# Kernel tuning notes

Hardware: AMD Instinct MI355X
Metric: run time of the kernel (lower is better)

The kernel has to match this reference:

```python
import jax, jax.numpy as jnp
import numpy as np

T, N, C, L, H, NL = 32, 16, 64, 64, 128, 128
NA = 2 * L              # action logits come from the K gather -> 2*L slots
TOTAL = 3 + H + NA + L  # packed RecurrentState width: a,p,v,h,a_probs,p_probs


def _gru_cell(x, h, Wih, Whh, bih, bhh):
    # PyTorch GRUCell math
    gi = x @ Wih.T + bih
    gh = h @ Whh.T + bhh
    i_r, i_z, i_n = jnp.split(gi, 3, axis=-1)
    h_r, h_z, h_n = jnp.split(gh, 3, axis=-1)
    r = jax.nn.sigmoid(i_r + h_r)
    z = jax.nn.sigmoid(i_z + h_z)
    n = jnp.tanh(i_n + r * h_n)
    return (1.0 - z) * n + z * h


def _gru_seq(xs, Wih, Whh, bih, bhh):
    # xs: (steps, B, H) -> outputs (steps, B, H), zero initial state (torch default)
    h0 = jnp.zeros((xs.shape[1], Whh.shape[1]), xs.dtype)
    def step(h, x):
        hn = _gru_cell(x, h, Wih, Whh, bih, bhh)
        return hn, hn
    _, out = jax.lax.scan(step, h0, xs)
    return out


def _forward(cond, rnn_hxs, emb, aemb, tg_Wih_f, tg_Whh_f, tg_bih_f, tg_bhh_f, tg_Wih_b, tg_Whh_b, tg_bih_b, tg_bhh_b, gc_Wih, gc_Whh, gc_bih, gc_bhh, f_W0, f_b0, f_W1, f_b1, f_W2, f_b2, c_W0, c_b0, c_W1, c_b1, c_W2, c_b2, a_W0, a_b0, a_W1, a_b1, a_Wc, a_bc, lines_obs, given_a, given_p):
    relu = jax.nn.relu
    hx = rnn_hxs[0]                       # (N, TOTAL): a(1) p(1) v(1) h(H) a_probs(NA) p_probs(L)
    h0 = hx[:, 3:3 + H]
    a_init = hx[:, 0].astype(jnp.int32)   # A[-1] = hx.a (zeros at episode start)

    # --- bidirectional task encoder over all L cyclic rolls of line embeddings ---
    M = emb[lines_obs[0]]                 # (N, L, H); only t=0 lines are used
    gi = jnp.transpose(M, (1, 0, 2))      # (L, N, H)
    j = jnp.arange(L)
    idx = (j[None, :] - j[:, None]) % L   # rolled[i, j] = gi[(j - i) % L]  (torch.roll)
    rolled = gi[idx]                      # (L_roll, L, N, H)

    def bidir(xs):
        of = _gru_seq(xs, tg_Wih_f, tg_Whh_f, tg_bih_f, tg_bhh_f)
        ob = _gru_seq(xs[::-1], tg_Wih_b, tg_Whh_b, tg_bih_b, tg_bhh_b)[::-1]
        return jnp.concatenate([of, ob], axis=-1)

    S = jax.vmap(bidir)(rolled)           # (L, L, N, 2H)
    K = S.reshape(L, L, N, 2, H).transpose(2, 0, 1, 3, 4).reshape(N, L, 2 * L, H)

    # --- time-batched MLPs (independent of recurrent state) ---
    q_all = relu(relu(relu(cond @ f_W0 + f_b0) @ f_W1 + f_b1) @ f_W2 + f_b2)   # (T,N,H)
    all_inputs = jnp.concatenate([cond, lines_obs.astype(cond.dtype)], axis=-1)
    v_all = relu(relu(all_inputs @ c_W0 + c_b0) @ c_W1 + c_b1) @ c_W2 + c_b2   # (T,N,1)

    a_prev = jnp.concatenate([a_init[None], given_a[:-1]], axis=0)             # A[t-1] per step
    Rn = jnp.arange(N)

    def step(h, inp):
        ap, pt, qt = inp
        hn = _gru_cell(aemb[ap], h, gc_Wih, gc_Whh, gc_bih, gc_bhh)
        x = relu(hn @ a_W0 + a_b0)
        x = relu(x @ a_W1 + a_b1)
        p_probs = jax.nn.softmax(x @ a_Wc + a_bc, axis=-1)                     # (N, L)
        k = K[Rn, pt]                                                          # (N, 2L, H)
        a_probs = jax.nn.softmax(jnp.einsum('nkh,nh->nk', k, qt), axis=-1)     # (N, 2L)
        return hn, (a_probs, p_probs)

    _, (a_probs, p_probs) = jax.lax.scan(step, h0, (a_prev, given_p, q_all))

    # original yields hx.h (the INITIAL hidden) at every step -- faithful to source
    h_rep = jnp.broadcast_to(h0[None], (T, N, H))
    hx_out = jnp.concatenate([
        given_a.astype(cond.dtype)[..., None],
        given_p.astype(cond.dtype)[..., None],
        v_all, h_rep, a_probs, p_probs], axis=-1)                              # (T, N, TOTAL)
    return hx_out


def setup_inputs():
    ki = iter(jax.random.split(jax.random.key(0), 48))
    def nrm(shape, s):
        return jax.random.normal(next(ki), shape, jnp.float32) * s
    sH = float(1.0 / np.sqrt(H))
    inp = {}
    inp["cond"] = jax.random.normal(next(ki), (T, N, C), jnp.float32)
    inp["lines_obs"] = jax.random.randint(next(ki), (T, N, L), 0, NL, jnp.int32)
    inp["given_a"] = jax.random.randint(next(ki), (T, N), 0, NA, jnp.int32)
    inp["given_p"] = jax.random.randint(next(ki), (T, N), 0, L, jnp.int32)
    inp["rnn_hxs"] = jnp.zeros((1, N, TOTAL), jnp.float32)
    inp["emb"] = nrm((NL, H), 1.0)
    inp["aemb"] = nrm((NA, H), 1.0)
    for nm in ("tg_Wih_f", "tg_Whh_f", "tg_Wih_b", "tg_Whh_b", "gc_Wih", "gc_Whh"):
        inp[nm] = nrm((3 * H, H), sH)
    for nm in ("tg_bih_f", "tg_bhh_f", "tg_bih_b", "tg_bhh_b", "gc_bih", "gc_bhh"):
        inp[nm] = nrm((3 * H,), sH)
    inp["f_W0"] = nrm((C, H), float(1.0 / np.sqrt(C))); inp["f_b0"] = jnp.zeros((H,), jnp.float32)
    inp["f_W1"] = nrm((H, H), sH); inp["f_b1"] = jnp.zeros((H,), jnp.float32)
    inp["f_W2"] = nrm((H, H), sH); inp["f_b2"] = jnp.zeros((H,), jnp.float32)
    Din = C + L
    inp["c_W0"] = nrm((Din, H), float(1.0 / np.sqrt(Din))); inp["c_b0"] = jnp.zeros((H,), jnp.float32)
    inp["c_W1"] = nrm((H, H), sH); inp["c_b1"] = jnp.zeros((H,), jnp.float32)
    inp["c_W2"] = nrm((H, 1), sH); inp["c_b2"] = jnp.zeros((1,), jnp.float32)
    inp["a_W0"] = nrm((H, H), sH); inp["a_b0"] = jnp.zeros((H,), jnp.float32)
    inp["a_W1"] = nrm((H, H), sH); inp["a_b1"] = jnp.zeros((H,), jnp.float32)
    inp["a_Wc"] = nrm((H, L), sH); inp["a_bc"] = jnp.zeros((L,), jnp.float32)
    return inp


def reference(cond, lines_obs, given_a, given_p, rnn_hxs, emb, aemb, tg_Wih_f, tg_Whh_f, tg_bih_f, tg_bhh_f, tg_Wih_b, tg_Whh_b, tg_bih_b, tg_bhh_b, gc_Wih, gc_Whh, gc_bih, gc_bhh, f_W0, f_b0, f_W1, f_b1, f_W2, f_b2, c_W0, c_b0, c_W1, c_b1, c_W2, c_b2, a_W0, a_b0, a_W1, a_b1, a_Wc, a_bc):
    hx_out = _forward(cond, rnn_hxs, emb, aemb, tg_Wih_f, tg_Whh_f, tg_bih_f, tg_bhh_f, tg_Wih_b, tg_Whh_b, tg_bih_b, tg_bhh_b, gc_Wih, gc_Whh, gc_bih, gc_bhh, f_W0, f_b0, f_W1, f_b1, f_W2, f_b2, c_W0, c_b0, c_W1, c_b1, c_W2, c_b2, a_W0, a_b0, a_W1, a_b1, a_Wc, a_bc, lines_obs, given_a, given_p)
    return (hx_out, hx_out[-1:])
```

## Files before the change

### kernel.cpp

```cpp
#include <hip/hip_runtime.h>
#include <hip/hip_bf16.h>

#define T_ 32
#define N_ 16
#define C_ 64
#define L_ 64
#define H_ 128
#define G3 384
#define TOT 323

#define OFF_XF 0
#define OFF_XB 393216
#define OFF_XG 786432
#define OFF_Q  983040
#define OFF_V  1048576
#define OFF_HS 1049088
#define KM_OFF 4458496

typedef __attribute__((ext_vector_type(8))) short s16x8;
typedef __attribute__((ext_vector_type(4))) short s16x4;
typedef __attribute__((ext_vector_type(4))) float fx4;

__device__ __forceinline__ unsigned short f2bf(float f) {
  unsigned u = __builtin_bit_cast(unsigned, f);
  unsigned r = (u + 0x7FFFu + ((u >> 16) & 1u)) >> 16;
  return (unsigned short)r;
}
__device__ __forceinline__ float bf2f(unsigned short u) {
  unsigned v = ((unsigned)u) << 16;
  return __builtin_bit_cast(float, v);
}
__device__ __forceinline__ float sigm(float x) {
  return __builtin_amdgcn_rcpf(1.f + __expf(-x));
}
__device__ __forceinline__ float tanh_(float x) {
  return 1.f - 2.f * __builtin_amdgcn_rcpf(__expf(2.f * x) + 1.f);
}

__global__ __launch_bounds__(512) void pre_kernel(
    const float* __restrict__ cond, const int* __restrict__ lines,
    const int* __restrict__ given_a, const float* __restrict__ hx,
    const float* __restrict__ emb, const float* __restrict__ aemb,
    const float* __restrict__ Wih_f, const float* __restrict__ bih_f,
    const float* __restrict__ Wih_b, const float* __restrict__ bih_b,
    const float* __restrict__ gc_Wih, const float* __restrict__ gc_bih,
    const float* __restrict__ f_W0, const float* __restrict__ f_b0,
    const float* __restrict__ f_W1, const float* __restrict__ f_b1,
    const float* __restrict__ f_W2, const float* __restrict__ f_b2,
    const float* __restrict__ c_W0, const float* __restrict__ c_b0,
    const float* __restrict__ c_W1, const float* __restrict__ c_b1,
    const float* __restrict__ c_W2, const float* __restrict__ c_b2,
    float* __restrict__ wsf)
{
  __shared__ __align__(16) float xs[2048];
  const int bid = blockIdx.x, tid = threadIdx.x;

  if (bid < 160) {
    unsigned short* xbf = (unsigned short*)xs;
    const float* W; const float* bias; float* outp;
    {
      int n = tid >> 5, k4 = (tid & 31) * 4;
      const float* src;
      if (bid < 128) {
        int l = bid >> 1;
        int e = lines[n * L_ + l];
        src = emb + e * H_ + k4;
      } else {
        int t = bid - 128;
        int ap = (t == 0) ? (int)hx[n * TOT] : given_a[(t - 1) * N_ + n];
        src = aemb + ap * H_ + k4;
      }
      float4 v = *(const float4*)src;
      s16x4 pk;
      pk[0] = (short)f2bf(v.x); pk[1] = (short)f2bf(v.y);
      pk[2] = (short)f2bf(v.z); pk[3] = (short)f2bf(v.w);
      int byte = (n * 256 + k4 * 2) ^ ((n & 7) << 4);
      *(s16x4*)((char*)xbf + byte) = pk;
    }
    if (bid < 128) {
      int d = bid & 1, l = bid >> 1;
      W = d ? Wih_b : Wih_f;  bias = d ? bih_b : bih_f;
      outp = wsf + (d ? OFF_XB : OFF_XF) + l * (G3 * N_);
    } else {
      W = gc_Wih; bias = gc_bih;
      outp = wsf + OFF_XG + (bid - 128) * (G3 * N_);
    }
    __syncthreads();
    const int w = tid >> 6, lane = tid & 63;
    const int col16 = lane & 15, krow = lane >> 4, bq = krow * 4;
    s16x8 Af[4];
    #pragma unroll
    for (int kb = 0; kb < 4; ++kb) {
      int ab = (col16 * 256 + kb * 64 + krow * 16) ^ ((col16 & 7) << 4);
      Af[kb] = *(const s16x8*)((const char*)xbf + ab);
    }
    #pragma unroll
    for (int g = 0; g < 3; ++g) {
      int cg = (g * 8 + w) * 16 + col16;
      float bv = bias[cg];
      fx4 a; a[0] = bv; a[1] = bv; a[2] = bv; a[3] = bv;
      #pragma unroll
      for (int kb = 0; kb < 4; ++kb) {
        const float* src = W + cg * H_ + kb * 32 + krow * 8;
        float4 aa = *(const float4*)src;
        float4 bb = *(const float4*)(src + 4);
        s16x8 sv;
        sv[0] = (short)f2bf(aa.x); sv[1] = (short)f2bf(aa.y);
        sv[2] = (short)f2bf(aa.z); sv[3] = (short)f2bf(aa.w);
        sv[4] = (short)f2bf(bb.x); sv[5] = (short)f2bf(bb.y);
        sv[6] = (short)f2bf(bb.z); sv[7] = (short)f2bf(bb.w);
        a = __builtin_amdgcn_mfma_f32_16x16x32_bf16(Af[kb], sv, a, 0, 0, 0);
      }
      #pragma unroll
      for (int r = 0; r < 4; ++r)
        outp[cg * 16 + bq + r] = a[r];
    }
  } else {
    const int grp = tid >> 7, c = tid & 127;
    const int tn = (bid - 160) * 4 + grp;
    const int lane = c & 63, widg = c >> 6;
    float* x0 = xs + grp * 384;
    float* x1 = x0 + 128;
    float* x2 = x0 + 256;
    float* xred = xs + 1536;
    if (c < 64) x0[c] = cond[tn * C_ + c];
    __syncthreads();
    {
      float a0 = f_b0[c], a1 = 0.f, a2 = 0.f, a3 = 0.f;
      #pragma unroll 4
      for (int k = 0; k < 64; k += 4) {
        a0 += x0[k] * f_W0[k * H_ + c];
        a1 += x0[k + 1] * f_W0[(k + 1) * H_ + c];
        a2 += x0[k + 2] * f_W0[(k + 2) * H_ + c];
        a3 += x0[k + 3] * f_W0[(k + 3) * H_ + c];
      }
      x1[c] = fmaxf((a0 + a1) + (a2 + a3), 0.f);
    }
    __syncthreads();
    {
      float a0 = f_b1[c], a1 = 0.f, a2 = 0.f, a3 = 0.f;
      #pragma unroll 4
      for (int k = 0; k < 128; k += 4) {
        a0 += x1[k] * f_W1[k * H_ + c];
        a1 += x1[k + 1] * f_W1[(k + 1) * H_ + c];
        a2 += x1[k + 2] * f_W1[(k + 2) * H_ + c];
        a3 += x1[k + 3] * f_W1[(k + 3) * H_ + c];
      }
      x2[c] = fmaxf((a0 + a1) + (a2 + a3), 0.f);
    }
    __syncthreads();
    {
      float a0 = f_b2[c], a1 = 0.f, a2 = 0.f, a3 = 0.f;
      #pragma unroll 4
      for (int k = 0; k < 128; k += 4) {
        a0 += x2[k] * f_W2[k * H_ + c];
        a1 += x2[k + 1] * f_W2[(k + 1) * H_ + c];
        a2 += x2[k + 2] * f_W2[(k + 2) * H_ + c];
        a3 += x2[k + 3] * f_W2[(k + 3) * H_ + c];
      }
      wsf[OFF_Q + tn * H_ + c] = fmaxf((a0 + a1) + (a2 + a3), 0.f);
    }
    __syncthreads();
    if (c < 64) {
      x0[c] = cond[tn * C_ + c];
      x0[64 + c] = (float)lines[tn * L_ + c];
    }
    __syncthreads();
    {
      float a0 = c_b0[c], a1 = 0.f, a2 = 0.f, a3 = 0.f;
      #pragma unroll 4
      for (int k = 0; k < 128; k += 4) {
        a0 += x0[k] * c_W0[k * H_ + c];
        a1 += x0[k + 1] * c_W0[(k + 1) * H_ + c];
        a2 += x0[k + 2] * c_W0[(k + 2) * H_ + c];
        a3 += x0[k + 3] * c_W0[(k + 3) * H_ + c];
      }
      x1[c] = fmaxf((a0 + a1) + (a2 + a3), 0.f);
    }
    __syncthreads();
    {
      float a0 = c_b1[c], a1 = 0.f, a2 = 0.f, a3 = 0.f;
      #pragma unroll 4
      for (int k = 0; k < 128; k += 4) {
        a0 += x1[k] * c_W1[k * H_ + c];
        a1 += x1[k + 1] * c_W1[(k + 1) * H_ + c];
        a2 += x1[k + 2] * c_W1[(k + 2) * H_ + c];
        a3 += x1[k + 3] * c_W1[(k + 3) * H_ + c];
      }
      x2[c] = fmaxf((a0 + a1) + (a2 + a3), 0.f);
    }
    __syncthreads();
    {
      float pv = x2[c] * c_W2[c];
      #pragma unroll
      for (int off = 32; off; off >>= 1) pv += __shfl_xor(pv, off);
      if (lane == 0) xred[grp * 2 + widg] = pv;
    }
    __syncthreads();
    if (c == 0)
      wsf[OFF_V + tn] = c_b2[0] + xred[grp * 2] + xred[grp * 2 + 1];
  }
}

__global__ __launch_bounds__(512) void mid_kernel(
    const float* __restrict__ Whh_f, const float* __restrict__ Whh_b,
    const float* __restrict__ bhh_f, const float* __restrict__ bhh_b,
    const float* __restrict__ gc_Whh, const float* __restrict__ gc_bhh,
    const float* __restrict__ hx,
    float* __restrict__ wsf, unsigned short* __restrict__ Km)
{
  __shared__ __align__(16) unsigned short hls[8192];
  const int bid = blockIdx.x, tid = threadIdx.x;

  if (bid < 64) {
    const int i = bid;
    const int wv = tid >> 6, lane = tid & 63;
    const int d = wv >> 2, ws4 = wv & 3;
    const int col16 = lane & 15, krow = lane >> 4, bq = krow * 4;
    const float* Whh = d ? Whh_b : Whh_f;
    const float* bhh = d ? bhh_b : bhh_f;
    const float* Xd = wsf + (d ? OFF_XB : OFF_XF);

    for (int idx = tid; idx < 8192; idx += 512) hls[idx] = 0;

    s16x8 Bf[3][2][4];
    float bias[3][2];
    int voff[3][2];
    #pragma unroll
    for (int g = 0; g < 3; ++g)
      #pragma unroll
      for (int tl = 0; tl < 2; ++tl) {
        int cg = g * 128 + ws4 * 32 + tl * 16 + col16;
        bias[g][tl] = bhh[cg];
        voff[g][tl] = cg * 16 + bq;
        #pragma unroll
        for (int kb = 0; kb < 4; ++kb) {
          const float* src = Whh + cg * H_ + kb * 32 + krow * 8;
          float4 aa = *(const float4*)src;
          float4 bb = *(const float4*)(src + 4);
          s16x8 sv;
          sv[0] = (short)f2bf(aa.x); sv[1] = (short)f2bf(aa.y);
          sv[2] = (short)f2bf(aa.z); sv[3] = (short)f2bf(aa.w);
          sv[4] = (short)f2bf(bb.x); sv[5] = (short)f2bf(bb.y);
          sv[6] = (short)f2bf(bb.z); sv[7] = (short)f2bf(bb.w);
          Bf[g][tl][kb] = sv;
        }
      }
    const int cc0 = ws4 * 32 + col16;
    const int jj0 = d ? 63 : 0;
    int koff[2][4];
    #pragma unroll
    for (int tl = 0; tl < 2; ++tl)
      #pragma unroll
      for (int r = 0; r < 4; ++r) {
        int b = bq + r, cc = cc0 + tl * 16;
        koff[tl][r] = (((b * 64 + i) * 128 + (2 * jj0 + d)) * 128 + cc) * 2;
      }
    const int kdel = d ? -512 : 512;
    float hreg[2][4] = {{0.f, 0.f, 0.f, 0.f}, {0.f, 0.f, 0.f, 0.f}};
    char* lb = (char*)hls + d * 8192;
    int lx = (jj0 - i) & 63;
    __syncthreads();

    fx4 xpA[3][2], xpB[3][2];
    {
      const float* Xc = Xd + lx * (G3 * N_);
      #pragma unroll
      for (int g = 0; g < 3; ++g)
        #pragma unroll
        for (int tl = 0; tl < 2; ++tl)
          xpA[g][tl] = *(const fx4*)(Xc + voff[g][tl]);
    }

    auto STEP = [&](int p, fx4 (&XC)[3][2], fx4 (&XN)[3][2]) {
      s16x8 Af[4];
      #pragma unroll
      for (int kb = 0; kb < 4; ++kb) {
        int ab = (col16 * 256 + kb * 64 + krow * 16) ^ ((col16 & 7) << 4);
        Af[kb] = *(const s16x8*)(lb + p * 4096 + ab);
      }
      int lxn = (d ? (lx - 1) : (lx + 1)) & 63;
      {
        const float* Xn = Xd + lxn * (G3 * N_);
        #pragma unroll
        for (int g = 0; g < 3; ++g)
          #pragma unroll
          for (int tl = 0; tl < 2; ++tl)
            XN[g][tl] = *(const fx4*)(Xn + voff[g][tl]);
      }
      fx4 acc[3][2];
      #pragma unroll
      for (int g = 0; g < 3; ++g)
        #pragma unroll
        for (int tl = 0; tl < 2; ++tl) {
          float bv = bias[g][tl];
          fx4 a; a[0] = bv; a[1] = bv; a[2] = bv; a[3] = bv;
          #pragma unroll
          for (int kb = 0; kb < 4; ++kb)
            a = __builtin_amdgcn_mfma_f32_16x16x32_bf16(Af[kb], Bf[g][tl][kb], a, 0, 0, 0);
          acc[g][tl] = a;
        }
      char* wb = lb + (p ^ 1) * 4096;
      unsigned short uu[2][4];
      #pragma unroll
      for (int tl = 0; tl < 2; ++tl) {
        int ccb = (cc0 + tl * 16) * 2;
        #pragma unroll
        for (int r = 0; r < 4; ++r) {
          int b = bq + r;
          float rr = sigm(XC[0][tl][r] + acc[0][tl][r]);
          float zz = sigm(XC[1][tl][r] + acc[1][tl][r]);
          float nn = tanh_(XC[2][tl][r] + rr * acc[2][tl][r]);
          float hn = nn + zz * (hreg[tl][r] - nn);
          hreg[tl][r] = hn;
          unsigned short u = f2bf(hn);
          uu[tl][r] = u;
          *(unsigned short*)(wb + ((b * 256 + ccb) ^ ((b & 7) << 4))) = u;
        }
      }
      #pragma unroll
      for (int tl = 0; tl < 2; ++tl)
        #pragma unroll
        for (int r = 0; r < 4; ++r) {
          *(unsigned short*)((char*)Km + koff[tl][r]) = uu[tl][r];
          koff[tl][r] += kdel;
        }
      asm volatile("s_waitcnt lgkmcnt(0)" ::: "memory");
      __builtin_amdgcn_s_barrier();
      asm volatile("" ::: "memory");
      lx = lxn;
    };

    #pragma unroll 1
    for (int it = 0; it < 32; ++it) {
      STEP(0, xpA, xpB);
      STEP(1, xpB, xpA);
    }
  } else {
    const int n = bid - 64;
    float* hcur = (float*)hls;
    float* gh = ((float*)hls) + 128;
    float4 wreg[32];
    float bias_ = 0.f;
    if (tid < 384) {
      const float4* wr = (const float4*)(gc_Whh + tid * H_);
      #pragma unroll
      for (int k4 = 0; k4 < 32; ++k4) wreg[k4] = wr[k4];
      bias_ = gc_bhh[tid];
    }
    if (tid < 128) hcur[tid] = hx[n * TOT + 3 + tid];
    __syncthreads();
    #pragma unroll 1
    for (int t = 0; t < 32; ++t) {
      if (tid < 384) {
        float a0 = bias_, a1 = 0.f, a2 = 0.f, a3 = 0.f;
        const float4* hv = (const float4*)hcur;
        #pragma unroll
        for (int k4 = 0; k4 < 32; k4 += 4) {
          float4 w0 = wreg[k4],     h0 = hv[k4];
          float4 w1 = wreg[k4 + 1], h1 = hv[k4 + 1];
          float4 w2 = wreg[k4 + 2], h2 = hv[k4 + 2];
          float4 w3 = wreg[k4 + 3], h3 = hv[k4 + 3];
          a0 += w0.x * h0.x + w0.y * h0.y + w0.z * h0.z + w0.w * h0.w;
          a1 += w1.x * h1.x + w1.y * h1.y + w1.z * h1.z + w1.w * h1.w;
          a2 += w2.x * h2.x + w2.y * h2.y + w2.z * h2.z + w2.w * h2.w;
          a3 += w3.x * h3.x + w3.y * h3.y + w3.z * h3.z + w3.w * h3.w;
        }
        gh[tid] = (a0 + a1) + (a2 + a3);
      }
      __syncthreads();
      if (tid < 128) {
        const float* xgt = wsf + OFF_XG + t * (G3 * N_);
        float rr = sigm(xgt[tid * 16 + n] + gh[tid]);
        float zz = sigm(xgt[(128 + tid) * 16 + n] + gh[128 + tid]);
        float nn = tanh_(xgt[(256 + tid) * 16 + n] + rr * gh[256 + tid]);
        float hn = nn + zz * (hcur[tid] - nn);
        hcur[tid] = hn;
        wsf[OFF_HS + (t * N_ + n) * H_ + tid] = hn;
      }
      __syncthreads();
    }
  }
}

__global__ __launch_bounds__(128) void post_kernel(
    const int* __restrict__ given_a, const int* __restrict__ given_p,
    const float* __restrict__ hx,
    const float* __restrict__ a_W0, const float* __restrict__ a_b0,
    const float* __restrict__ a_W1, const float* __restrict__ a_b1,
    const float* __restrict__ a_Wc, const float* __restrict__ a_bc,
    const float* __restrict__ wsf, const unsigned short* __restrict__ Km,
    float* __restrict__ out)
{
  __shared__ __align__(16) unsigned short ktile[16384];
  __shared__ float xa[128], xb2[128], qv[128], red[4];
  const int tn = blockIdx.x, t = tn >> 4, n = tn & 15;
  const int c = threadIdx.x;
  const int lane = c & 63, wid = c >> 6;

  {
    int pt = given_p[tn];
    const s16x8* src = (const s16x8*)(Km + (n * 64 + pt) * 16384);
    #pragma unroll
    for (int it = 0; it < 16; ++it) {
      int chunk = it * 128 + c;
      s16x8 v = src[chunk];
      int byte = chunk * 16;
      int row = byte >> 8;
      *(s16x8*)((char*)ktile + (byte ^ ((row & 7) << 4))) = v;
    }
  }
  xa[c] = wsf[OFF_HS + tn * H_ + c];
  qv[c] = wsf[OFF_Q + tn * H_ + c];
  __syncthreads();
  float s = a_b0[c];
  #pragma unroll 8
  for (int k = 0; k < 128; ++k) s += xa[k] * a_W0[k * H_ + c];
  xb2[c] = fmaxf(s, 0.f);
  __syncthreads();
  s = a_b1[c];
  #pragma unroll 8
  for (int k = 0; k < 128; ++k) s += xb2[k] * a_W1[k * H_ + c];
  float x2v = fmaxf(s, 0.f);
  __syncthreads();
  xa[c] = x2v;
  __syncthreads();
  float al = 0.f;
  #pragma unroll
  for (int k8 = 0; k8 < 16; ++k8) {
    int byte = c * 256 + k8 * 16;
    s16x8 kv = *(const s16x8*)((const char*)ktile + (byte ^ ((c & 7) << 4)));
    #pragma unroll
    for (int j = 0; j < 8; ++j)
      al += bf2f((unsigned short)kv[j]) * qv[k8 * 8 + j];
  }
  float pl = 0.f;
  if (wid == 0) {
    float s2 = a_bc[lane];
    #pragma unroll 8
    for (int k = 0; k < 128; ++k) s2 += xa[k] * a_Wc[k * 64 + lane];
    pl = s2;
  }
  float m = al;
  #pragma unroll
  for (int off = 32; off; off >>= 1) m = fmaxf(m, __shfl_xor(m, off));
  if (lane == 0) red[wid] = m;
  __syncthreads();
  m = fmaxf(red[0], red[1]);
  float e = __expf(al - m);
  float ssum = e;
  #pragma unroll
  for (int off = 32; off; off >>= 1) ssum += __shfl_xor(ssum, off);
  if (lane == 0) red[2 + wid] = ssum;
  __syncthreads();
  float ap = e * __builtin_amdgcn_rcpf(red[2] + red[3]);

  const int obase = tn * TOT;
  const bool tail = (t == 31);
  const int tbase = 512 * TOT + n * TOT;
  out[obase + 131 + c] = ap;
  if (tail) out[tbase + 131 + c] = ap;
  {
    float hv = hx[n * TOT + 3 + c];
    out[obase + 3 + c] = hv;
    if (tail) out[tbase + 3 + c] = hv;
  }
  if (wid == 0) {
    float pm = pl;
    #pragma unroll
    for (int off = 32; off; off >>= 1) pm = fmaxf(pm, __shfl_xor(pm, off));
    float pe = __expf(pl - pm);
    float ps = pe;
    #pragma unroll
    for (int off = 32; off; off >>= 1) ps += __shfl_xor(ps, off);
    float pp = pe * __builtin_amdgcn_rcpf(ps);
    out[obase + 259 + lane] = pp;
    if (tail) out[tbase + 259 + lane] = pp;
  }
  if (c == 0) {
    float u0 = (float)given_a[tn];
    float u1 = (float)given_p[tn];
    float u2 = wsf[OFF_V + tn];
    out[obase + 0] = u0; out[obase + 1] = u1; out[obase + 2] = u2;
    if (tail) { out[tbase + 0] = u0; out[tbase + 1] = u1; out[tbase + 2] = u2; }
  }
}

extern "C" void kernel_launch(void* const* d_in, const int* in_sizes, int n_in,
                              void* d_out, int out_size, void* d_ws, size_t ws_size,
                              hipStream_t stream) {
  const float* cond  = (const float*)d_in[0];
  const int*   lines = (const int*)d_in[1];
  const int*   ga    = (const int*)d_in[2];
  const int*   gp    = (const int*)d_in[3];
  const float* hx    = (const float*)d_in[4];
  const float* emb   = (const float*)d_in[5];
  const float* aemb  = (const float*)d_in[6];
  const float* Wih_f = (const float*)d_in[7];
  const float* Whh_f = (const float*)d_in[8];
  const float* Wih_b = (const float*)d_in[9];
  const float* Whh_b = (const float*)d_in[10];
  const float* gcWih = (const float*)d_in[11];
  const float* gcWhh = (const float*)d_in[12];
  const float* bih_f = (const float*)d_in[13];
  const float* bhh_f = (const float*)d_in[14];
  const float* bih_b = (const float*)d_in[15];
  const float* bhh_b = (const float*)d_in[16];
  const float* gcbih = (const float*)d_in[17];
  const float* gcbhh = (const float*)d_in[18];
  const float* f_W0 = (const float*)d_in[19]; const float* f_b0 = (const float*)d_in[20];
  const float* f_W1 = (const float*)d_in[21]; const float* f_b1 = (const float*)d_in[22];
  const float* f_W2 = (const float*)d_in[23]; const float* f_b2 = (const float*)d_in[24];
  const float* c_W0 = (const float*)d_in[25]; const float* c_b0 = (const float*)d_in[26];
  const float* c_W1 = (const float*)d_in[27]; const float* c_b1 = (const float*)d_in[28];
  const float* c_W2 = (const float*)d_in[29]; const float* c_b2 = (const float*)d_in[30];
  const float* a_W0 = (const float*)d_in[31]; const float* a_b0 = (const float*)d_in[32];
  const float* a_W1 = (const float*)d_in[33]; const float* a_b1 = (const float*)d_in[34];
  const float* a_Wc = (const float*)d_in[35]; const float* a_bc = (const float*)d_in[36];

  float* wsf = (float*)d_ws;
  unsigned short* Km = (unsigned short*)((char*)d_ws + KM_OFF);
  float* out = (float*)d_out;

  pre_kernel<<<288, 512, 0, stream>>>(cond, lines, ga, hx, emb, aemb,
      Wih_f, bih_f, Wih_b, bih_b, gcWih, gcbih,
      f_W0, f_b0, f_W1, f_b1, f_W2, f_b2,
      c_W0, c_b0, c_W1, c_b1, c_W2, c_b2, wsf);
  mid_kernel<<<80, 512, 0, stream>>>(Whh_f, Whh_b, bhh_f, bhh_b,
      gcWhh, gcbhh, hx, wsf, Km);
  post_kernel<<<512, 128, 0, stream>>>(ga, gp, hx,
      a_W0, a_b0, a_W1, a_b1, a_Wc, a_bc, wsf, Km, out);
}
```

Before: 257.0 us.

## Split bidirectional GRU across separate blocks and read K rows directly in post

The mid kernel now gives each (roll, direction) pair its own block of 8 waves instead of packing both directions into one 512-thread block. Each wave handles a single 16-column tile per gate, which halves the serial MFMA and gate work per recurrence step and doubles the block count to use more CUs. The post kernel drops its LDS staging of the K tile and reads each K row straight from global memory, issuing that dot product before the MLP. The pre kernel writes its MFMA output as a single vector store. The cost is more blocks and fewer registers held per wave, and the post kernel's global reads are per-row strided rather than coalesced into LDS.

```diff
diff --git a/kernel.cpp b/kernel.cpp
--- a/kernel.cpp
+++ b/kernel.cpp
@@ -111,9 +111,7 @@
         sv[6] = (short)f2bf(bb.z); sv[7] = (short)f2bf(bb.w);
         a = __builtin_amdgcn_mfma_f32_16x16x32_bf16(Af[kb], sv, a, 0, 0, 0);
       }
-      #pragma unroll
-      for (int r = 0; r < 4; ++r)
-        outp[cg * 16 + bq + r] = a[r];
+      *(fx4*)(outp + cg * 16 + bq) = a;
     }
   } else {
     const int grp = tid >> 7, c = tid & 127;
@@ -209,122 +207,96 @@
     const float* __restrict__ hx,
     float* __restrict__ wsf, unsigned short* __restrict__ Km)
 {
-  __shared__ __align__(16) unsigned short hls[8192];
+  __shared__ __align__(16) unsigned short hls[4096];
   const int bid = blockIdx.x, tid = threadIdx.x;
 
-  if (bid < 64) {
-    const int i = bid;
-    const int wv = tid >> 6, lane = tid & 63;
-    const int d = wv >> 2, ws4 = wv & 3;
-    const int col16 = lane & 15, krow = lane >> 4, bq = krow * 4;
+  if (bid < 128) {
+    const int i = bid >> 1, d = bid & 1;
     const float* Whh = d ? Whh_b : Whh_f;
     const float* bhh = d ? bhh_b : bhh_f;
     const float* Xd = wsf + (d ? OFF_XB : OFF_XF);
-
-    for (int idx = tid; idx < 8192; idx += 512) hls[idx] = 0;
-
-    s16x8 Bf[3][2][4];
-    float bias[3][2];
-    int voff[3][2];
-    #pragma unroll
-    for (int g = 0; g < 3; ++g)
-      #pragma unroll
-      for (int tl = 0; tl < 2; ++tl) {
-        int cg = g * 128 + ws4 * 32 + tl * 16 + col16;
-        bias[g][tl] = bhh[cg];
-        voff[g][tl] = cg * 16 + bq;
-        #pragma unroll
-        for (int kb = 0; kb < 4; ++kb) {
-          const float* src = Whh + cg * H_ + kb * 32 + krow * 8;
-          float4 aa = *(const float4*)src;
-          float4 bb = *(const float4*)(src + 4);
-          s16x8 sv;
-          sv[0] = (short)f2bf(aa.x); sv[1] = (short)f2bf(aa.y);
-          sv[2] = (short)f2bf(aa.z); sv[3] = (short)f2bf(aa.w);
-          sv[4] = (short)f2bf(bb.x); sv[5] = (short)f2bf(bb.y);
-          sv[6] = (short)f2bf(bb.z); sv[7] = (short)f2bf(bb.w);
-          Bf[g][tl][kb] = sv;
-        }
-      }
-    const int cc0 = ws4 * 32 + col16;
+    const int w = tid >> 6, lane = tid & 63;
+    const int col16 = lane & 15, krow = lane >> 4, bq = krow * 4;
+    const int cc = w * 16 + col16;
+
+    for (int idx = tid; idx < 4096; idx += 512) hls[idx] = 0;
+
+    s16x8 Bf[3][4];
+    float bias[3];
+    int voff[3];
+    #pragma unroll
+    for (int g = 0; g < 3; ++g) {
+      int cg = (g * 8 + w) * 16 + col16;
+      bias[g] = bhh[cg];
+      voff[g] = cg * 16 + bq;
+      #pragma unroll
+      for (int kb = 0; kb < 4; ++kb) {
+        const float* src = Whh + cg * H_ + kb * 32 + krow * 8;
+        float4 aa = *(const float4*)src;
+        float4 bb = *(const float4*)(src + 4);
+        s16x8 sv;
+        sv[0] = (short)f2bf(aa.x); sv[1] = (short)f2bf(aa.y);
+        sv[2] = (short)f2bf(aa.z); sv[3] = (short)f2bf(aa.w);
+        sv[4] = (short)f2bf(bb.x); sv[5] = (short)f2bf(bb.y);
+        sv[6] = (short)f2bf(bb.z); sv[7] = (short)f2bf(bb.w);
+        Bf[g][kb] = sv;
+      }
+    }
     const int jj0 = d ? 63 : 0;
-    int koff[2][4];
-    #pragma unroll
-    for (int tl = 0; tl < 2; ++tl)
-      #pragma unroll
-      for (int r = 0; r < 4; ++r) {
-        int b = bq + r, cc = cc0 + tl * 16;
-        koff[tl][r] = (((b * 64 + i) * 128 + (2 * jj0 + d)) * 128 + cc) * 2;
-      }
+    int koff[4];
+    #pragma unroll
+    for (int r = 0; r < 4; ++r)
+      koff[r] = ((((bq + r) * 64 + i) * 128 + (2 * jj0 + d)) * 128 + cc) * 2;
     const int kdel = d ? -512 : 512;
-    float hreg[2][4] = {{0.f, 0.f, 0.f, 0.f}, {0.f, 0.f, 0.f, 0.f}};
-    char* lb = (char*)hls + d * 8192;
+    float hreg[4] = {0.f, 0.f, 0.f, 0.f};
+    char* lbase = (char*)hls;
     int lx = (jj0 - i) & 63;
     __syncthreads();
 
-    fx4 xpA[3][2], xpB[3][2];
+    fx4 xpA[3], xpB[3];
     {
       const float* Xc = Xd + lx * (G3 * N_);
       #pragma unroll
-      for (int g = 0; g < 3; ++g)
-        #pragma unroll
-        for (int tl = 0; tl < 2; ++tl)
-          xpA[g][tl] = *(const fx4*)(Xc + voff[g][tl]);
-    }
-
-    auto STEP = [&](int p, fx4 (&XC)[3][2], fx4 (&XN)[3][2]) {
+      for (int g = 0; g < 3; ++g) xpA[g] = *(const fx4*)(Xc + voff[g]);
+    }
+
+    auto STEP = [&](int p, fx4 (&XC)[3], fx4 (&XN)[3]) {
       s16x8 Af[4];
       #pragma unroll
       for (int kb = 0; kb < 4; ++kb) {
         int ab = (col16 * 256 + kb * 64 + krow * 16) ^ ((col16 & 7) << 4);
-        Af[kb] = *(const s16x8*)(lb + p * 4096 + ab);
+        Af[kb] = *(const s16x8*)(lbase + p * 4096 + ab);
       }
       int lxn = (d ? (lx - 1) : (lx + 1)) & 63;
       {
         const float* Xn = Xd + lxn * (G3 * N_);
         #pragma unroll
-        for (int g = 0; g < 3; ++g)
-          #pragma unroll
-          for (int tl = 0; tl < 2; ++tl)
-            XN[g][tl] = *(const fx4*)(Xn + voff[g][tl]);
-      }
-      fx4 acc[3][2];
-      #pragma unroll
-      for (int g = 0; g < 3; ++g)
+        for (int g = 0; g < 3; ++g) XN[g] = *(const fx4*)(Xn + voff[g]);
+      }
+      fx4 acc[3];
+      #pragma unroll
+      for (int g = 0; g < 3; ++g) {
+        float bv = bias[g];
+        fx4 a; a[0] = bv; a[1] = bv; a[2] = bv; a[3] = bv;
         #pragma unroll
-        for (int tl = 0; tl < 2; ++tl) {
-          float bv = bias[g][tl];
-          fx4 a; a[0] = bv; a[1] = bv; a[2] = bv; a[3] = bv;
-          #pragma unroll
-          for (int kb = 0; kb < 4; ++kb)
-            a = __builtin_amdgcn_mfma_f32_16x16x32_bf16(Af[kb], Bf[g][tl][kb], a, 0, 0, 0);
-          acc[g][tl] = a;
-        }
-      char* wb = lb + (p ^ 1) * 4096;
-      unsigned short uu[2][4];
-      #pragma unroll
-      for (int tl = 0; tl < 2; ++tl) {
-        int ccb = (cc0 + tl * 16) * 2;
-        #pragma unroll
-        for (int r = 0; r < 4; ++r) {
-          int b = bq + r;
-          float rr = sigm(XC[0][tl][r] + acc[0][tl][r]);
-          float zz = sigm(XC[1][tl][r] + acc[1][tl][r]);
-          float nn = tanh_(XC[2][tl][r] + rr * acc[2][tl][r]);
-          float hn = nn + zz * (hreg[tl][r] - nn);
-          hreg[tl][r] = hn;
-          unsigned short u = f2bf(hn);
-          uu[tl][r] = u;
-          *(unsigned short*)(wb + ((b * 256 + ccb) ^ ((b & 7) << 4))) = u;
-        }
-      }
-      #pragma unroll
-      for (int tl = 0; tl < 2; ++tl)
-        #pragma unroll
-        for (int r = 0; r < 4; ++r) {
-          *(unsigned short*)((char*)Km + koff[tl][r]) = uu[tl][r];
-          koff[tl][r] += kdel;
-        }
+        for (int kb = 0; kb < 4; ++kb)
+          a = __builtin_amdgcn_mfma_f32_16x16x32_bf16(Af[kb], Bf[g][kb], a, 0, 0, 0);
+        acc[g] = a;
+      }
+      char* wbb = lbase + (p ^ 1) * 4096;
+      #pragma unroll
+      for (int r = 0; r < 4; ++r) {
+        int b = bq + r;
+        float rr = sigm(XC[0][r] + acc[0][r]);
+        float zz = sigm(XC[1][r] + acc[1][r]);
+        float nn = tanh_(XC[2][r] + rr * acc[2][r]);
+        float hn = nn + zz * (hreg[r] - nn);
+        hreg[r] = hn;
+        unsigned short u = f2bf(hn);
+        *(unsigned short*)(wbb + ((b * 256 + cc * 2) ^ ((b & 7) << 4))) = u;
+        *(unsigned short*)((char*)Km + koff[r]) = u;
+        koff[r] += kdel;
+      }
       asm volatile("s_waitcnt lgkmcnt(0)" ::: "memory");
       __builtin_amdgcn_s_barrier();
       asm volatile("" ::: "memory");
@@ -337,7 +309,7 @@
       STEP(1, xpB, xpA);
     }
   } else {
-    const int n = bid - 64;
+    const int n = bid - 128;
     float* hcur = (float*)hls;
     float* gh = ((float*)hls) + 128;
     float4 wreg[32];
@@ -392,27 +364,27 @@
     const float* __restrict__ wsf, const unsigned short* __restrict__ Km,
     float* __restrict__ out)
 {
-  __shared__ __align__(16) unsigned short ktile[16384];
   __shared__ float xa[128], xb2[128], qv[128], red[4];
   const int tn = blockIdx.x, t = tn >> 4, n = tn & 15;
   const int c = threadIdx.x;
   const int lane = c & 63, wid = c >> 6;
 
-  {
-    int pt = given_p[tn];
-    const s16x8* src = (const s16x8*)(Km + (n * 64 + pt) * 16384);
-    #pragma unroll
-    for (int it = 0; it < 16; ++it) {
-      int chunk = it * 128 + c;
-      s16x8 v = src[chunk];
-      int byte = chunk * 16;
-      int row = byte >> 8;
-      *(s16x8*)((char*)ktile + (byte ^ ((row & 7) << 4))) = v;
-    }
-  }
+  const int pt = given_p[tn];
+  const unsigned short* krow_ = Km + ((n * 64 + pt) * 128 + c) * 128;
+
   xa[c] = wsf[OFF_HS + tn * H_ + c];
   qv[c] = wsf[OFF_Q + tn * H_ + c];
   __syncthreads();
+
+  float al = 0.f;
+  #pragma unroll
+  for (int k8 = 0; k8 < 16; ++k8) {
+    s16x8 kv = *(const s16x8*)(krow_ + k8 * 8);
+    #pragma unroll
+    for (int j = 0; j < 8; ++j)
+      al += bf2f((unsigned short)kv[j]) * qv[k8 * 8 + j];
+  }
+
   float s = a_b0[c];
   #pragma unroll 8
   for (int k = 0; k < 128; ++k) s += xa[k] * a_W0[k * H_ + c];
@@ -425,15 +397,6 @@
   __syncthreads();
   xa[c] = x2v;
   __syncthreads();
-  float al = 0.f;
-  #pragma unroll
-  for (int k8 = 0; k8 < 16; ++k8) {
-    int byte = c * 256 + k8 * 16;
-    s16x8 kv = *(const s16x8*)((const char*)ktile + (byte ^ ((c & 7) << 4)));
-    #pragma unroll
-    for (int j = 0; j < 8; ++j)
-      al += bf2f((unsigned short)kv[j]) * qv[k8 * 8 + j];
-  }
   float pl = 0.f;
   if (wid == 0) {
     float s2 = a_bc[lane];
@@ -526,7 +489,7 @@
       Wih_f, bih_f, Wih_b, bih_b, gcWih, gcbih,
       f_W0, f_b0, f_W1, f_b1, f_W2, f_b2,
       c_W0, c_b0, c_W1, c_b1, c_W2, c_b2, wsf);
-  mid_kernel<<<80, 512, 0, stream>>>(Whh_f, Whh_b, bhh_f, bhh_b,
+  mid_kernel<<<144, 512, 0, stream>>>(Whh_f, Whh_b, bhh_f, bhh_b,
       gcWhh, gcbhh, hx, wsf, Km);
   post_kernel<<<512, 128, 0, stream>>>(ga, gp, hx,
       a_W0, a_b0, a_W1, a_b1, a_Wc, a_bc, wsf, Km, out);
```

Result: faster. 216.4 us (-15.8%).
